# Kernel tuning notes

Hardware: AMD Instinct MI355X
Metric: run time of the kernel (lower is better)

Reference implementation:

```python
import jax, jax.numpy as jnp
import numpy as np

T, B, D, H = 256, 128, 512, 512  # seq_len, batch, input_dim, hidden_dim (= n_qubits)


def setup_inputs() -> dict:
    key = jax.random.key(0)
    ks = jax.random.split(key, 17)
    s = 0.02
    inp = {"inputs": jax.random.normal(ks[0], (T, B, D), dtype=jnp.float32)}
    for j, n in enumerate(["f", "i", "u", "o"]):
        inp["W" + n] = jax.random.normal(ks[1 + 4 * j], (D + H, H), dtype=jnp.float32) * s
        inp["b" + n] = jnp.zeros((H,), jnp.float32)
        inp["rx" + n] = jax.random.normal(ks[2 + 4 * j], (H,), dtype=jnp.float32)
        inp["P" + n] = jax.random.normal(ks[3 + 4 * j], (H, H), dtype=jnp.float32) * s
    return inp


def _qlayer(z, rx, P):
    # per-wire trainable rotation RX(theta) acting on the scalar feature of each
    # wire (scales it by cos(theta)), followed by the bias-free `pre` linear.
    return (z * jnp.cos(rx)) @ P


def reference(inputs, Wf, bf, Wi, bi, Wu, bu, Wo, bo, rxf, rxi, rxu, rxo, Pf, Pi, Pu, Po):
    Bc, Hc = inputs.shape[1], bf.shape[0]

    def step(carry, x_t):
        hx, cx = carry
        comb = jnp.concatenate([x_t, hx], axis=1)  # (B, D+H)
        f = jax.nn.sigmoid(_qlayer(comb @ Wf + bf, rxf, Pf))
        i = jax.nn.sigmoid(_qlayer(comb @ Wi + bi, rxi, Pi))
        g = jnp.tanh(_qlayer(comb @ Wu + bu, rxu, Pu))
        o = jax.nn.sigmoid(_qlayer(comb @ Wo + bo, rxo, Po))
        cx = f * cx + i * g
        hx = o * jnp.tanh(cx)
        return (hx, cx), hx

    h0 = jnp.zeros((Bc, Hc), inputs.dtype)
    (hx, cx), outputs = jax.lax.scan(step, (h0, h0), inputs)
    return outputs, hx, cx
```

## Files before the change

kernel.cpp:

```cpp
#include <hip/hip_runtime.h>
#include <hip/hip_bf16.h>

typedef __attribute__((ext_vector_type(8))) short bf16x8;
typedef __attribute__((ext_vector_type(4))) float f32x4;
typedef __attribute__((ext_vector_type(4))) unsigned int u32x4;
typedef unsigned short u16;
typedef unsigned int u32;

#define SENT 0x7FC07FC0u

__device__ __forceinline__ u16 f2bf(float f) {
  union { float f; unsigned u; } v; v.f = f;
  unsigned r = v.u + 0x7FFFu + ((v.u >> 16) & 1u);
  return (u16)(r >> 16);
}

__device__ __forceinline__ float sigm_fast(float x) {
  return __builtin_amdgcn_rcpf(1.f + __expf(-x));
}
__device__ __forceinline__ float tanh_fast(float x) {
  x = fminf(fmaxf(x, -15.f), 15.f);
  float e = __expf(2.f * x);
  return (e - 1.f) * __builtin_amdgcn_rcpf(e + 1.f);
}

__device__ __forceinline__ void ld_llc_b128(const u16* p, bf16x8& r) {
  asm volatile("global_load_dwordx4 %0, %1, off sc0 sc1" : "=&v"(r) : "v"(p));
}
__device__ __forceinline__ void ld_g_b128(const u16* p, bf16x8& r) {
  asm volatile("global_load_dwordx4 %0, %1, off" : "=&v"(r) : "v"(p));
}
__device__ __forceinline__ void st_llc_b128(u16* p, u32x4 v) {
  asm volatile("global_store_dwordx4 %0, %1, off sc0 sc1" :: "v"(p), "v"(v) : "memory");
}
__device__ __forceinline__ void st_g_b32(u32* p, u32 v) {
  asm volatile("global_store_dword %0, %1, off" :: "v"(p), "v"(v) : "memory");
}

__global__ __launch_bounds__(256) void fold_kernel(
    const float* __restrict__ W0, const float* __restrict__ rx0, const float* __restrict__ P0,
    const float* __restrict__ W1, const float* __restrict__ rx1, const float* __restrict__ P1,
    const float* __restrict__ W2, const float* __restrict__ rx2, const float* __restrict__ P2,
    const float* __restrict__ W3, const float* __restrict__ rx3, const float* __restrict__ P3,
    u16* __restrict__ Wt)
{
  const int g = blockIdx.z;
  const float* W  = (g == 0) ? W0  : (g == 1) ? W1  : (g == 2) ? W2  : W3;
  const float* rx = (g == 0) ? rx0 : (g == 1) ? rx1 : (g == 2) ? rx2 : rx3;
  const float* P  = (g == 0) ? P0  : (g == 1) ? P1  : (g == 2) ? P2  : P3;
  __shared__ __align__(16) float As[16][68];
  __shared__ __align__(16) float Bs[16][68];
  const int bk = blockIdx.x, bj = blockIdx.y;
  const int tid = threadIdx.x;
  const int tx = tid & 15, ty = tid >> 4;
  const int j0 = bj * 64, k0 = bk * 64;
  float acc[4][4] = {};
  for (int m0 = 0; m0 < 512; m0 += 16) {
#pragma unroll
    for (int l = 0; l < 4; ++l) {
      int lin = tid + 256 * l;
      int mm = lin >> 6, jr = lin & 63;
      As[mm][jr] = P[(m0 + mm) * 512 + j0 + jr];
      int kk = lin >> 4, mb = lin & 15;
      Bs[mb][kk] = W[(k0 + kk) * 512 + m0 + mb] * cosf(rx[m0 + mb]);
    }
    __syncthreads();
#pragma unroll
    for (int mm = 0; mm < 16; ++mm) {
      f32x4 a = *(const f32x4*)&As[mm][ty * 4];
      f32x4 b = *(const f32x4*)&Bs[mm][tx * 4];
#pragma unroll
      for (int i = 0; i < 4; ++i)
#pragma unroll
        for (int jj = 0; jj < 4; ++jj)
          acc[i][jj] += a[i] * b[jj];
    }
    __syncthreads();
  }
#pragma unroll
  for (int i = 0; i < 4; ++i) {
    int j = j0 + ty * 4 + i;
    size_t n = (size_t)(j * 4 + g);
    ushort4 w;
    w.x = f2bf(acc[i][0]); w.y = f2bf(acc[i][1]);
    w.z = f2bf(acc[i][2]); w.w = f2bf(acc[i][3]);
    *(ushort4*)(Wt + n * 1024 + k0 + tx * 4) = w;
  }
}

__global__ __launch_bounds__(256) void fold_bias(
    const float* __restrict__ b0, const float* __restrict__ rx0, const float* __restrict__ P0,
    const float* __restrict__ b1, const float* __restrict__ rx1, const float* __restrict__ P1,
    const float* __restrict__ b2, const float* __restrict__ rx2, const float* __restrict__ P2,
    const float* __restrict__ b3, const float* __restrict__ rx3, const float* __restrict__ P3,
    float* __restrict__ bpn)
{
  const int g = blockIdx.x >> 3, jb = blockIdx.x & 7;
  const float* b  = (g == 0) ? b0  : (g == 1) ? b1  : (g == 2) ? b2  : b3;
  const float* rx = (g == 0) ? rx0 : (g == 1) ? rx1 : (g == 2) ? rx2 : rx3;
  const float* P  = (g == 0) ? P0  : (g == 1) ? P1  : (g == 2) ? P2  : P3;
  __shared__ float bc[512];
  __shared__ float red[4][65];
  const int tid = threadIdx.x;
  bc[tid] = b[tid] * cosf(rx[tid]);
  bc[tid + 256] = b[tid + 256] * cosf(rx[tid + 256]);
  __syncthreads();
  const int jl = tid & 63, msub = tid >> 6;
  const int j = jb * 64 + jl;
  float acc = 0.f;
  for (int m = msub * 128; m < msub * 128 + 128; ++m)
    acc += bc[m] * P[m * 512 + j];
  red[msub][jl] = acc;
  __syncthreads();
  if (msub == 0)
    bpn[j * 4 + g] = red[0][jl] + red[1][jl] + red[2][jl] + red[3][jl];
}

__global__ __launch_bounds__(256) void xcvt_kernel(
    const float* __restrict__ x, u16* __restrict__ xb)
{
  size_t i = (size_t)blockIdx.x * 256 + threadIdx.x;
  f32x4 v = *(const f32x4*)(x + i * 4);
  ushort4 w;
  w.x = f2bf(v[0]); w.y = f2bf(v[1]); w.z = f2bf(v[2]); w.w = f2bf(v[3]);
  *(ushort4*)(xb + i * 4) = w;
}

__global__ __launch_bounds__(256) void init_kernel(u32* hslab32, u32* hz32,
                                                   float* cbuf) {
  int i = blockIdx.x * 256 + threadIdx.x;
  hslab32[i] = SENT;
  hslab32[i + 65536] = SENT;
  hz32[i] = 0;
  cbuf[i] = 0.f;
}

__global__ __launch_bounds__(256) void tail_kernel(
    const float* __restrict__ hlast, const float* __restrict__ c,
    float* __restrict__ hx, float* __restrict__ cx)
{
  int i = blockIdx.x * 256 + threadIdx.x;
  hx[i] = hlast[i];
  cx[i] = c[i];
}

__global__ __launch_bounds__(256) void step_kernel(
    const u16* __restrict__ xb_t, const u16* __restrict__ h_in,
    u16* __restrict__ h_out, const u16* __restrict__ Wt,
    const float* __restrict__ bpn, float* __restrict__ cbuf,
    float* __restrict__ out_t)
{
  __shared__ float pre_s[32][33];
  const int bid = blockIdx.x;
  const int mb = bid >> 6, nb = bid & 63;
  const int b0 = mb * 32, n0 = nb * 32;
  const int tid = threadIdx.x;
  const int wv = tid >> 6, lane = tid & 63;
  const int rt = wv >> 1, nt = wv & 1;
  const int l15 = lane & 15, kg = lane >> 4;
  const int brow = b0 + rt * 16 + l15;
  const int ncol = n0 + nt * 16 + l15;
  const u16* wrow = Wt + (size_t)ncol * 1024;
  const u16* xrow = xb_t + (size_t)brow * 512;
  const u16* hrow = h_in + (size_t)brow * 512;
  f32x4 acc = {0.f, 0.f, 0.f, 0.f};
#pragma unroll 8
  for (int kk = 0; kk < 32; ++kk) {
    const int kb = kk * 32 + kg * 8;
    bf16x8 bfrag = *(const bf16x8*)(wrow + kb);
    bf16x8 afrag;
    if (kb < 512) afrag = *(const bf16x8*)(xrow + kb);
    else          afrag = *(const bf16x8*)(hrow + (kb - 512));
    acc = __builtin_amdgcn_mfma_f32_16x16x32_bf16(afrag, bfrag, acc, 0, 0, 0);
  }
  const float bias = bpn[ncol];
#pragma unroll
  for (int q = 0; q < 4; ++q)
    pre_s[rt * 16 + kg * 4 + q][nt * 16 + l15] = acc[q] + bias;
  __syncthreads();
  const int bb = tid >> 3, jo = tid & 7;
  float pf = pre_s[bb][jo * 4 + 0];
  float pi = pre_s[bb][jo * 4 + 1];
  float pu = pre_s[bb][jo * 4 + 2];
  float po = pre_s[bb][jo * 4 + 3];
  float fg = 1.f / (1.f + __expf(-pf));
  float ig = 1.f / (1.f + __expf(-pi));
  float gg = tanhf(pu);
  float og = 1.f / (1.f + __expf(-po));
  size_t idx = (size_t)(b0 + bb) * 512 + (size_t)(nb * 8 + jo);
  float cv = fg * cbuf[idx] + ig * gg;
  cbuf[idx] = cv;
  float hv = og * tanhf(cv);
  out_t[idx] = hv;
  h_out[idx] = f2bf(hv);
}

__global__ __launch_bounds__(256, 1) void qlstm_persistent(
    const u16* __restrict__ Xbf,
    u16* __restrict__ hslab,
    const u16* __restrict__ Wt,
    const float* __restrict__ bpn,
    float* __restrict__ out)
{
  __shared__ float pre_s[2][32][33];
  const int bid = blockIdx.x;
  const int mb = bid & 3, nb = bid >> 2;
  const int b0 = mb * 32, n0 = nb * 32;
  const int tid = threadIdx.x;
  const int wv = tid >> 6, lane = tid & 63;
  const int rt = wv >> 1, nt = wv & 1;
  const int l15 = lane & 15, kg = lane >> 4;
  const int brow = b0 + rt * 16 + l15;
  const int ncol = n0 + nt * 16 + l15;

  const u16* wrow = Wt + (size_t)ncol * 1024;
  bf16x8 warr[32];
#pragma unroll
  for (int kk = 0; kk < 32; ++kk)
    warr[kk] = *(const bf16x8*)(wrow + kk * 32 + kg * 8);
  const float bnc = bpn[ncol];

  const int bb = tid >> 3, jo = tid & 7;
  const size_t eidx = (size_t)(b0 + bb) * 512 + (size_t)(nb * 8 + jo);
  const bool pst = ((tid & 7) == 0);
  const size_t prow_off = (size_t)(b0 + (tid >> 3)) * 512 + (size_t)(nb * 8);
  const u32x4 sentv = {SENT, SENT, SENT, SENT};
  float cst = 0.f, hl = 0.f;

  bf16x8 xf[16];
  {
    const u16* xr = Xbf + (size_t)brow * 512;
#pragma unroll
    for (int kk = 0; kk < 16; ++kk)
      ld_g_b128(xr + kk * 32 + kg * 8, xf[kk]);
    asm volatile("s_waitcnt vmcnt(0)" ::: "memory");
  }

  for (int t = 0; t < 256; ++t) {
    const u16* hr = hslab + (size_t)(t & 3) * 65536 + (size_t)brow * 512;
    bf16x8 hf[16];
    if (t > 0) {
#pragma unroll
      for (int kk = 0; kk < 16; ++kk)
        ld_llc_b128(hr + kk * 32 + kg * 8, hf[kk]);
    }
    asm volatile("s_waitcnt vmcnt(16)" ::: "memory");
    __builtin_amdgcn_sched_barrier(0);

    f32x4 ax0 = {0,0,0,0}, ax1 = {0,0,0,0};
#pragma unroll
    for (int kk = 0; kk < 16; kk += 2) {
      ax0 = __builtin_amdgcn_mfma_f32_16x16x32_bf16(xf[kk],     warr[kk],     ax0, 0, 0, 0);
      ax1 = __builtin_amdgcn_mfma_f32_16x16x32_bf16(xf[kk + 1], warr[kk + 1], ax1, 0, 0, 0);
    }

    f32x4 ah0 = {0,0,0,0}, ah1 = {0,0,0,0};
    if (t > 0) {
      int guard = 0;
      for (;;) {
        asm volatile("s_waitcnt vmcnt(0)" ::: "memory");
        __builtin_amdgcn_sched_barrier(0);
        u32 bad = 0;
#pragma unroll
        for (int kk = 0; kk < 16; ++kk) {
          union { bf16x8 v; u32 d[4]; } u; u.v = hf[kk];
          bad |= (u.d[0] == SENT) | (u.d[1] == SENT)
               | (u.d[2] == SENT) | (u.d[3] == SENT);
        }
        if (__all((int)(bad == 0))) break;
        if (++guard > 30000) break;
        __builtin_amdgcn_s_sleep(1);
#pragma unroll
        for (int kk = 0; kk < 16; ++kk)
          ld_llc_b128(hr + kk * 32 + kg * 8, hf[kk]);
      }
      __builtin_amdgcn_sched_barrier(0);
#pragma unroll
      for (int kk = 0; kk < 16; kk += 2) {
        ah0 = __builtin_amdgcn_mfma_f32_16x16x32_bf16(hf[kk],     warr[16 + kk],     ah0, 0, 0, 0);
        ah1 = __builtin_amdgcn_mfma_f32_16x16x32_bf16(hf[kk + 1], warr[16 + kk + 1], ah1, 0, 0, 0);
      }
    }
    f32x4 acc = (ax0 + ax1) + (ah0 + ah1);

    if (pst)
      st_llc_b128(hslab + (size_t)((t + 2) & 3) * 65536 + prow_off, sentv);

#pragma unroll
    for (int q = 0; q < 4; ++q)
      pre_s[t & 1][rt * 16 + kg * 4 + q][nt * 16 + l15] = acc[q] + bnc;
    asm volatile("s_waitcnt lgkmcnt(0)" ::: "memory");
    __builtin_amdgcn_sched_barrier(0);
    __builtin_amdgcn_s_barrier();
    asm volatile("" ::: "memory");

    float pf = pre_s[t & 1][bb][jo * 4 + 0];
    float pi = pre_s[t & 1][bb][jo * 4 + 1];
    float pu = pre_s[t & 1][bb][jo * 4 + 2];
    float po = pre_s[t & 1][bb][jo * 4 + 3];
    cst = sigm_fast(pf) * cst + sigm_fast(pi) * tanh_fast(pu);
    float hv = sigm_fast(po) * tanh_fast(cst);
    hl = hv;

    u16 myh = f2bf(hv);
    u32 w  = (u32)myh | ((u32)(u16)__shfl_xor((int)(u32)myh, 1) << 16);
    u32 d1 = (u32)__shfl_xor((int)w, 2);
    u32 d2 = (u32)__shfl_xor((int)w, 4);
    u32 d3 = (u32)__shfl_xor((int)w, 6);

    asm volatile("s_waitcnt vmcnt(0)" ::: "memory");
    if (pst) {
      u32x4 hw = {w, d1, d2, d3};
      st_llc_b128(hslab + (size_t)((t + 1) & 3) * 65536 + prow_off, hw);
    }
    union { float f; u32 u; } ho; ho.f = hv;
    st_g_b32((u32*)(out + (size_t)t * 65536 + eidx), ho.u);
    if (t < 255) {
      const u16* xr = Xbf + (size_t)(t + 1) * 65536 + (size_t)brow * 512;
#pragma unroll
      for (int kk = 0; kk < 16; ++kk)
        ld_g_b128(xr + kk * 32 + kg * 8, xf[kk]);
    }
  }

  asm volatile("s_waitcnt vmcnt(0)" ::: "memory");
  out[(size_t)256 * 65536 + eidx] = hl;
  out[(size_t)256 * 65536 + 65536 + eidx] = cst;
}

extern "C" void kernel_launch(void* const* d_in, const int* in_sizes, int n_in,
                              void* d_out, int out_size, void* d_ws, size_t ws_size,
                              hipStream_t stream) {
  (void)in_sizes; (void)n_in; (void)out_size; (void)ws_size;
  const float* inp = (const float*)d_in[0];
  float* out = (float*)d_out;

  char* base = (char*)d_ws;
  u16*   Xbf   = (u16*)base;
  u16*   Wt    = (u16*)(base + 33554432);
  float* bpn   = (float*)(base + 33554432 + 4194304);
  u16*   hslab = (u16*)(base + 33554432 + 4194304 + 8192);
  u16*   hz    = (u16*)(base + 33554432 + 4194304 + 8192 + 524288);
  float* cbuf  = (float*)(base + 33554432 + 4194304 + 8192 + 524288 + 262144);

  const float* W[4];  const float* b[4];  const float* rx[4];  const float* P[4];
  for (int g = 0; g < 4; ++g) {
    W[g]  = (const float*)d_in[1 + 4 * g];
    b[g]  = (const float*)d_in[2 + 4 * g];
    rx[g] = (const float*)d_in[3 + 4 * g];
    P[g]  = (const float*)d_in[4 + 4 * g];
  }
  fold_kernel<<<dim3(16, 8, 4), 256, 0, stream>>>(
      W[0], rx[0], P[0], W[1], rx[1], P[1],
      W[2], rx[2], P[2], W[3], rx[3], P[3], Wt);
  fold_bias<<<dim3(32), 256, 0, stream>>>(
      b[0], rx[0], P[0], b[1], rx[1], P[1],
      b[2], rx[2], P[2], b[3], rx[3], P[3], bpn);
  xcvt_kernel<<<16384, 256, 0, stream>>>(inp, Xbf);
  init_kernel<<<256, 256, 0, stream>>>((u32*)hslab, (u32*)hz, cbuf);

  void* args[5];
  const u16* Xbf_c = Xbf;
  const u16* Wt_c = Wt;
  const float* bpn_c = bpn;
  u16* hslab_p = hslab;
  float* out_p = out;
  args[0] = (void*)&Xbf_c;
  args[1] = (void*)&hslab_p;
  args[2] = (void*)&Wt_c;
  args[3] = (void*)&bpn_c;
  args[4] = (void*)&out_p;
  hipError_t e = hipLaunchCooperativeKernel((const void*)qlstm_persistent,
                                            dim3(256), dim3(256), args, 0, stream);
  if (e != hipSuccess) {
    for (int t = 0; t < 256; ++t) {
      const u16* xb_t  = Xbf + (size_t)t * 65536;
      const u16* h_in  = hz + (size_t)(t & 1) * 65536;
      u16*       h_oup = hz + (size_t)((t & 1) ^ 1) * 65536;
      float*     out_t = out + (size_t)t * 65536;
      step_kernel<<<256, 256, 0, stream>>>(xb_t, h_in, h_oup, Wt, bpn, cbuf, out_t);
    }
    tail_kernel<<<256, 256, 0, stream>>>(out + (size_t)255 * 65536, cbuf,
                                         out + (size_t)256 * 65536,
                                         out + (size_t)256 * 65536 + 65536);
  }
}
```

Measured before the change: 1.660 ms.

## Remove block barrier by computing gates per-wave and re-polling only stale chunks

Each wave now owns a 16x16 tile whose four interleaved gate columns sit in its own LDS slice. The gate combine is done inside the wave, so the block-wide s_barrier per timestep is removed and each wave publishes its own 4-column h slice with 64-bit stores. The spin-wait on the shared h slab now reloads only the 16-byte chunks that still hold the sentinel, and the poll guard limit is lowered. This takes intra-block synchronization off the recurrent critical path, but produces more, smaller h stores and the removed vmcnt wait before the store changes memory ordering.

```diff
diff --git a/kernel.cpp b/kernel.cpp
--- a/kernel.cpp
+++ b/kernel.cpp
@@ -4,6 +4,7 @@
 typedef __attribute__((ext_vector_type(8))) short bf16x8;
 typedef __attribute__((ext_vector_type(4))) float f32x4;
 typedef __attribute__((ext_vector_type(4))) unsigned int u32x4;
+typedef __attribute__((ext_vector_type(2))) unsigned int u32x2;
 typedef unsigned short u16;
 typedef unsigned int u32;
 
@@ -30,8 +31,8 @@
 __device__ __forceinline__ void ld_g_b128(const u16* p, bf16x8& r) {
   asm volatile("global_load_dwordx4 %0, %1, off" : "=&v"(r) : "v"(p));
 }
-__device__ __forceinline__ void st_llc_b128(u16* p, u32x4 v) {
-  asm volatile("global_store_dwordx4 %0, %1, off sc0 sc1" :: "v"(p), "v"(v) : "memory");
+__device__ __forceinline__ void st_llc_b64(u16* p, u32x2 v) {
+  asm volatile("global_store_dwordx2 %0, %1, off sc0 sc1" :: "v"(p), "v"(v) : "memory");
 }
 __device__ __forceinline__ void st_g_b32(u32* p, u32 v) {
   asm volatile("global_store_dword %0, %1, off" :: "v"(p), "v"(v) : "memory");
@@ -202,7 +203,7 @@
     const float* __restrict__ bpn,
     float* __restrict__ out)
 {
-  __shared__ float pre_s[2][32][33];
+  __shared__ float pre_s[4][16][17];
   const int bid = blockIdx.x;
   const int mb = bid & 3, nb = bid >> 2;
   const int b0 = mb * 32, n0 = nb * 32;
@@ -220,11 +221,9 @@
     warr[kk] = *(const bf16x8*)(wrow + kk * 32 + kg * 8);
   const float bnc = bpn[ncol];
 
-  const int bb = tid >> 3, jo = tid & 7;
-  const size_t eidx = (size_t)(b0 + bb) * 512 + (size_t)(nb * 8 + jo);
-  const bool pst = ((tid & 7) == 0);
-  const size_t prow_off = (size_t)(b0 + (tid >> 3)) * 512 + (size_t)(nb * 8);
-  const u32x4 sentv = {SENT, SENT, SENT, SENT};
+  const int jglob = nb * 8 + nt * 4 + kg;
+  const size_t eidx = (size_t)brow * 512 + (size_t)jglob;
+  const size_t hrow_off = (size_t)brow * 512 + (size_t)(nb * 8 + nt * 4);
   float cst = 0.f, hl = 0.f;
 
   bf16x8 xf[16];
@@ -256,23 +255,27 @@
 
     f32x4 ah0 = {0,0,0,0}, ah1 = {0,0,0,0};
     if (t > 0) {
+      asm volatile("s_waitcnt vmcnt(0)" ::: "memory");
+      __builtin_amdgcn_sched_barrier(0);
       int guard = 0;
       for (;;) {
+        u32 stale = 0;
+#pragma unroll
+        for (int kk = 0; kk < 16; ++kk) {
+          union { bf16x8 v; u32 d[4]; } u; u.v = hf[kk];
+          u32 s = (u32)((u.d[0] == SENT) | (u.d[1] == SENT) |
+                        (u.d[2] == SENT) | (u.d[3] == SENT));
+          stale |= s << kk;
+        }
+        if (__all((int)(stale == 0))) break;
+        if (++guard > 20000) break;
+        __builtin_amdgcn_s_sleep(1);
+#pragma unroll
+        for (int kk = 0; kk < 16; ++kk)
+          if ((stale >> kk) & 1)
+            ld_llc_b128(hr + kk * 32 + kg * 8, hf[kk]);
         asm volatile("s_waitcnt vmcnt(0)" ::: "memory");
         __builtin_amdgcn_sched_barrier(0);
-        u32 bad = 0;
-#pragma unroll
-        for (int kk = 0; kk < 16; ++kk) {
-          union { bf16x8 v; u32 d[4]; } u; u.v = hf[kk];
-          bad |= (u.d[0] == SENT) | (u.d[1] == SENT)
-               | (u.d[2] == SENT) | (u.d[3] == SENT);
-        }
-        if (__all((int)(bad == 0))) break;
-        if (++guard > 30000) break;
-        __builtin_amdgcn_s_sleep(1);
-#pragma unroll
-        for (int kk = 0; kk < 16; ++kk)
-          ld_llc_b128(hr + kk * 32 + kg * 8, hf[kk]);
       }
       __builtin_amdgcn_sched_barrier(0);
 #pragma unroll
@@ -283,36 +286,33 @@
     }
     f32x4 acc = (ax0 + ax1) + (ah0 + ah1);
 
-    if (pst)
-      st_llc_b128(hslab + (size_t)((t + 2) & 3) * 65536 + prow_off, sentv);
+    {
+      u32x2 sv = {SENT, SENT};
+      if (kg == 0)
+        st_llc_b64(hslab + (size_t)((t + 2) & 3) * 65536 + hrow_off, sv);
+    }
 
 #pragma unroll
     for (int q = 0; q < 4; ++q)
-      pre_s[t & 1][rt * 16 + kg * 4 + q][nt * 16 + l15] = acc[q] + bnc;
+      pre_s[wv][kg * 4 + q][l15] = acc[q] + bnc;
     asm volatile("s_waitcnt lgkmcnt(0)" ::: "memory");
     __builtin_amdgcn_sched_barrier(0);
-    __builtin_amdgcn_s_barrier();
-    asm volatile("" ::: "memory");
-
-    float pf = pre_s[t & 1][bb][jo * 4 + 0];
-    float pi = pre_s[t & 1][bb][jo * 4 + 1];
-    float pu = pre_s[t & 1][bb][jo * 4 + 2];
-    float po = pre_s[t & 1][bb][jo * 4 + 3];
-    cst = sigm_fast(pf) * cst + sigm_fast(pi) * tanh_fast(pu);
-    float hv = sigm_fast(po) * tanh_fast(cst);
+    f32x4 g4 = *(const f32x4*)&pre_s[wv][l15][kg * 4];
+    asm volatile("s_waitcnt lgkmcnt(0)" ::: "memory");
+    __builtin_amdgcn_sched_barrier(0);
+
+    cst = sigm_fast(g4[0]) * cst + sigm_fast(g4[1]) * tanh_fast(g4[2]);
+    float hv = sigm_fast(g4[3]) * tanh_fast(cst);
     hl = hv;
 
     u16 myh = f2bf(hv);
-    u32 w  = (u32)myh | ((u32)(u16)__shfl_xor((int)(u32)myh, 1) << 16);
-    u32 d1 = (u32)__shfl_xor((int)w, 2);
-    u32 d2 = (u32)__shfl_xor((int)w, 4);
-    u32 d3 = (u32)__shfl_xor((int)w, 6);
-
-    asm volatile("s_waitcnt vmcnt(0)" ::: "memory");
-    if (pst) {
-      u32x4 hw = {w, d1, d2, d3};
-      st_llc_b128(hslab + (size_t)((t + 1) & 3) * 65536 + prow_off, hw);
-    }
+    u32 w  = (u32)myh | ((u32)(u16)__shfl_xor((int)(u32)myh, 16) << 16);
+    u32 w2 = (u32)__shfl_xor((int)w, 32);
+    if (kg == 0) {
+      u32x2 hw = {w, w2};
+      st_llc_b64(hslab + (size_t)((t + 1) & 3) * 65536 + hrow_off, hw);
+    }
+
     union { float f; u32 u; } ho; ho.f = hv;
     st_g_b32((u32*)(out + (size_t)t * 65536 + eidx), ho.u);
     if (t < 255) {
```

New measurement: 2.772 ms. +67.0%, slower.
